# Performance work log

Measured on AMD Instinct MI355X. Metric: run time of the kernel, lower is better.

Reference implementation:

```python
import jax, jax.numpy as jnp
import numpy as np

# Dims (match init_kwargs / input_specs)
B, N, DIM, HEADS, DHEAD, CHUNK = 1, 2048, 1024, 8, 128, 64
HID = 4 * DHEAD            # MemoryMLP expansion_factor=4.0
DI = HEADS * DHEAD         # dim_inner
EPS = 1e-6
MAX_LR = 1.0               # default_step_transform_max_lr


def rmsnorm(x, w):
    return x * jax.lax.rsqrt(jnp.mean(jnp.square(x), -1, keepdims=True) + EPS) * w


def mem_forward(w0, w1, g, x):
    # ResidualNorm(MemoryMLP): y = RMSNorm(gelu(x@w0)@w1)*g + x
    h = jax.nn.gelu(x @ w0, approximate=False) @ w1
    return rmsnorm(h, g) + x


def setup_inputs() -> dict:
    key = jax.random.key(0)
    ks = jax.random.split(key, 12)
    s = lambda i, shape, sc: jax.random.normal(ks[i], shape, jnp.float32) * sc
    return dict(
        x=s(0, (B, N, DIM), 1.0),
        store_norm_w=jnp.ones((DIM,), jnp.float32),
        ret_norm_w=jnp.ones((DIM,), jnp.float32),
        Wq=s(1, (DIM, DI), DIM ** -0.5),
        Wk=s(2, (DIM, DI), DIM ** -0.5),
        Wv=s(3, (DIM, DI), DIM ** -0.5),
        W_step=s(4, (DIM, HEADS), DIM ** -0.5), b_step=jnp.zeros((HEADS,), jnp.float32),
        W_mom=s(5, (DIM, HEADS), DIM ** -0.5), b_mom=jnp.zeros((HEADS,), jnp.float32),
        W_decay=s(6, (DIM, HEADS), DIM ** -0.5), b_decay=jnp.zeros((HEADS,), jnp.float32),
        gate_W=s(7, (DIM, HEADS), DIM ** -0.5),
        combine_W=s(8, (DI, DIM), DI ** -0.5),
        mem_w0=s(9, (HEADS, DHEAD, HID), DHEAD ** -0.5),
        mem_w1=s(10, (HEADS, HID, DHEAD), HID ** -0.5),
        mem_g=jnp.ones((HEADS, DHEAD), jnp.float32),
    )


def reference(x, store_norm_w, ret_norm_w, Wq, Wk, Wv, W_step, b_step,
              W_mom, b_mom, W_decay, b_decay, gate_W, combine_W,
              mem_w0, mem_w1, mem_g):
    b, n, _ = x.shape
    nc = n // CHUNK
    BH = b * HEADS

    # ---- store path ----
    s = rmsnorm(x, store_norm_w)                                 # b n dim
    lr = jax.nn.sigmoid(s @ W_step + b_step) * MAX_LR            # b n h (per-token adaptive step)
    pooled = s.reshape(b, nc, CHUNK, DIM).mean(2)                # b nc dim (AveragePool chunk rep)
    mom = jax.nn.sigmoid(pooled @ W_mom + b_mom)                 # b nc h
    dec = jax.nn.sigmoid(pooled @ W_decay + b_decay)             # b nc h

    def to_chunks(t):  # b n (h d) -> (b h) nc c d
        return t.reshape(b, nc, CHUNK, HEADS, DHEAD).transpose(0, 3, 1, 2, 4).reshape(BH, nc, CHUNK, DHEAD)

    k = to_chunks(s @ Wk)
    v = to_chunks(s @ Wv)
    lr_c = lr.reshape(b, nc, CHUNK, HEADS).transpose(0, 3, 1, 2).reshape(BH, nc, CHUNK)
    mom_bh = mom.transpose(0, 2, 1).reshape(BH, nc)
    dec_bh = dec.transpose(0, 2, 1).reshape(BH, nc)

    # init fast weights per (b h)  (per_head_learned_parameters=True)
    w0 = jnp.broadcast_to(mem_w0[None], (b, HEADS, DHEAD, HID)).reshape(BH, DHEAD, HID)
    w1 = jnp.broadcast_to(mem_w1[None], (b, HEADS, HID, DHEAD)).reshape(BH, HID, DHEAD)
    g = jnp.broadcast_to(mem_g[None], (b, HEADS, DHEAD)).reshape(BH, DHEAD)

    def chunk_loss(w0_, w1_, g_, kc, vc, lrc):
        pred = mem_forward(w0_, w1_, g_, kc)                     # c d
        return jnp.sum(jnp.mean(jnp.square(pred - vc), -1) * lrc)

    grad_chunk = jax.grad(chunk_loss, argnums=(0, 1, 2))
    # vmap over chunks (same weights per chunk, per-sample grads), then over (b h)
    grads = jax.vmap(jax.vmap(grad_chunk, in_axes=(None, None, None, 0, 0, 0)))(w0, w1, g, k, v, lr_c)
    surprises = tuple(-gr for gr in grads)                       # each (BH, nc, ...)

    def combine(a, c):
        ga, xa = a
        gb, xb = c
        return (ga * gb, gb * xa + xb)

    def lin_scan(gates, xs):
        # y_i = gates_i * y_{i-1} + xs_i over chunk axis (axis=1)
        return jax.lax.associative_scan(combine, (gates, xs), axis=1)

    def expand(gates, ref):
        return gates.reshape(gates.shape + (1,) * (ref.ndim - 2))

    # momentum scan per parameter tensor
    updates = tuple(lin_scan(expand(mom_bh, su), su)[1] for su in surprises)

    # weight update scan: W_i = (1 - decay_i) * W_{i-1} + momentum_i, W_{-1} = init
    per_chunk_weights = []
    for upd, w_init in zip(updates, (w0, w1, g)):
        gates = expand(1.0 - dec_bh, upd)
        cumg, y = lin_scan(gates, upd)
        w_seq = y + cumg * w_init[:, None]                       # (BH, nc, ...)
        # retrieval at chunk i uses weights updated through chunk i-1
        per_chunk_weights.append(jnp.concatenate([w_init[:, None], w_seq[:, :-1]], axis=1))
    w0_c, w1_c, g_c = per_chunk_weights

    # ---- retrieve path ----
    r = rmsnorm(x, ret_norm_w)
    q = to_chunks(r @ Wq)                                        # (BH, nc, c, d)
    pred = jax.vmap(jax.vmap(mem_forward))(w0_c, w1_c, g_c, q)   # (BH, nc, c, d)
    out = pred.reshape(b, HEADS, n, DHEAD)                       # b h n d
    gate = jax.nn.sigmoid(r @ gate_W)                            # b n h (retrieve_gate, heads>1)
    out = out * gate.transpose(0, 2, 1)[..., None]
    out = out.transpose(0, 2, 1, 3).reshape(b, n, DI) @ combine_W
    return out
```

## Files before the change

kernel.cpp:

```cpp
#include <hip/hip_runtime.h>
#include <hip/hip_bf16.h>
#include <math.h>

#define NH   8
#define DHD  128
#define HIDN 512
#define CHK  64
#define NCH  32
#define MB   1048576ull

typedef unsigned short u16;
typedef unsigned int   u32;
typedef short s16x8 __attribute__((ext_vector_type(8)));
typedef float f32x4 __attribute__((ext_vector_type(4)));

#define MFMA(a,b,c) __builtin_amdgcn_mfma_f32_16x16x32_bf16((a),(b),(c),0,0,0)

__device__ __forceinline__ float bf2f(u16 v){ return __uint_as_float(((u32)v) << 16); }
__device__ __forceinline__ u16 f2bf(float f){
  u32 u = __float_as_uint(f);
  u += 0x7fffu + ((u >> 16) & 1u);
  return (u16)(u >> 16);
}
__device__ __forceinline__ u32 pack2(float a, float b){
  return (u32)f2bf(a) | ((u32)f2bf(b) << 16);
}
__device__ __forceinline__ float dot2(u32 a, u32 b){
  return __uint_as_float(a << 16)*__uint_as_float(b << 16)
       + __uint_as_float(a & 0xffff0000u)*__uint_as_float(b & 0xffff0000u);
}
__device__ __forceinline__ float waveRedSum(float v){
  #pragma unroll
  for (int off = 32; off; off >>= 1) v += __shfl_xor(v, off);
  return v;
}
__device__ __forceinline__ void gload16(const void* g, void* l){
  __builtin_amdgcn_global_load_lds(
      (const __attribute__((address_space(1))) u32*)g,
      (__attribute__((address_space(3))) u32*)l, 16, 0, 0);
}
__device__ __forceinline__ int swzb(int row, int colb){ return colb ^ ((row & 7) << 4); }
__device__ __forceinline__ int swza(int row, int colb){
  return colb ^ ((row & 7) << 4) ^ (((row >> 3) & 3) << 5);
}



__global__ __launch_bounds__(256) void k_rmsnorm(const float* __restrict__ x,
    const float* __restrict__ wst, const float* __restrict__ wrt,
    u16* __restrict__ s_bf, u16* __restrict__ r_bf){
  int row = blockIdx.x, t = threadIdx.x;
  float4 v = ((const float4*)(x + (size_t)row*1024))[t];
  float ss = v.x*v.x + v.y*v.y + v.z*v.z + v.w*v.w;
  ss = waveRedSum(ss);
  __shared__ float red[4];
  int wv = t >> 6, ln = t & 63;
  if (ln == 0) red[wv] = ss;
  __syncthreads();
  float rr = rsqrtf((red[0]+red[1]+red[2]+red[3])*(1.f/1024.f) + 1e-6f);
  float4 a = ((const float4*)wst)[t];
  float4 b = ((const float4*)wrt)[t];
  uint2 so = make_uint2(pack2(v.x*rr*a.x, v.y*rr*a.y), pack2(v.z*rr*a.z, v.w*rr*a.w));
  uint2 ro = make_uint2(pack2(v.x*rr*b.x, v.y*rr*b.y), pack2(v.z*rr*b.z, v.w*rr*b.w));
  *(uint2*)(s_bf + (size_t)row*1024 + t*4) = so;
  *(uint2*)(r_bf + (size_t)row*1024 + t*4) = ro;
}

__global__ __launch_bounds__(256) void k_pool(const u16* __restrict__ s_bf, float* __restrict__ pooled){
  int c = blockIdx.x; int d = blockIdx.y*256 + threadIdx.x;
  float acc = 0.f;
  for (int tt = 0; tt < 64; ++tt) acc += bf2f(s_bf[((size_t)c*64+tt)*1024 + d]);
  pooled[(size_t)c*1024 + d] = acc * (1.f/64.f);
}

__global__ __launch_bounds__(256) void k_lrgate(const u16* __restrict__ s_bf, const u16* __restrict__ r_bf,
    const u16* __restrict__ WsgL, const float* __restrict__ bstep,
    float* __restrict__ lrc, float* __restrict__ gate){
  int wv = threadIdx.x >> 6, ln = threadIdx.x & 63;
  int tok = blockIdx.x*4 + wv;
  const u16* sp = s_bf + (size_t)tok*1024 + ln*16;
  const u16* rp = r_bf + (size_t)tok*1024 + ln*16;
  uint4 s0 = *(const uint4*)sp, s1 = *(const uint4*)(sp+8);
  uint4 r0 = *(const uint4*)rp, r1 = *(const uint4*)(rp+8);
  #pragma unroll 4
  for (int o = 0; o < 16; ++o){
    const u16* wp = WsgL + (size_t)o*1024 + ln*16;
    uint4 w0v = *(const uint4*)wp, w1v = *(const uint4*)(wp+8);
    uint4 a0 = (o < 8) ? s0 : r0, a1 = (o < 8) ? s1 : r1;
    float acc = dot2(a0.x,w0v.x)+dot2(a0.y,w0v.y)+dot2(a0.z,w0v.z)+dot2(a0.w,w0v.w)
              + dot2(a1.x,w1v.x)+dot2(a1.y,w1v.y)+dot2(a1.z,w1v.z)+dot2(a1.w,w1v.w);
    acc = waveRedSum(acc);
    if (ln == 0){
      int h = o & 7;
      if (o < 8){
        float v = 1.f/(1.f+expf(-(acc + bstep[h])));
        lrc[((size_t)h*NCH + (tok>>6))*CHK + (tok&63)] = v;
      } else {
        gate[(size_t)tok*8 + h] = 1.f/(1.f+expf(-acc));
      }
    }
  }
}

__global__ __launch_bounds__(64) void k_momdec(const float* __restrict__ pooled,
    const float* __restrict__ Wmom, const float* __restrict__ bmom,
    const float* __restrict__ Wdec, const float* __restrict__ bdec,
    float* __restrict__ momb, float* __restrict__ decb){
  int c = blockIdx.x, ln = threadIdx.x;
  const float* prow = pooled + (size_t)c*1024;
  for (int o = 0; o < 16; ++o){
    int h = o & 7;
    const float* W = (o < 8) ? Wmom : Wdec;
    float acc = 0.f;
    for (int k = ln; k < 1024; k += 64) acc += prow[k]*W[(size_t)k*8+h];
    acc = waveRedSum(acc);
    if (ln == 0){
      float bb = (o < 8) ? bmom[h] : bdec[h];
      float v = 1.f/(1.f+expf(-(acc+bb)));
      if (o < 8) momb[h*NCH + c] = v; else decb[h*NCH + c] = v;
    }
  }
}

__global__ __launch_bounds__(256) void k_trf4(
    const float* __restrict__ A0, const float* __restrict__ A1,
    const float* __restrict__ A2, const float* __restrict__ A3,
    u16* __restrict__ O0, u16* __restrict__ O1, u16* __restrict__ O2, u16* __restrict__ O3){
  __shared__ u16 tile[32][34];
  int z = blockIdx.z;
  const float* in = (z==0)?A0:(z==1)?A1:(z==2)?A2:A3;
  u16* out = (z==0)?O0:(z==1)?O1:(z==2)?O2:O3;
  int c0 = blockIdx.x*32, r0 = blockIdx.y*32;
  int tx = threadIdx.x & 31, ty = threadIdx.x >> 5;
  #pragma unroll
  for (int k = 0; k < 4; ++k) tile[ty+k*8][tx] = f2bf(in[(size_t)(r0+ty+k*8)*1024 + c0+tx]);
  __syncthreads();
  #pragma unroll
  for (int k = 0; k < 4; ++k) out[(size_t)(c0+ty+k*8)*1024 + r0+tx] = tile[tx][ty+k*8];
}

__global__ __launch_bounds__(256) void k_packw(const float* __restrict__ mw0, const float* __restrict__ mw1,
    const float* __restrict__ Wstep, const float* __restrict__ gateW,
    u16* __restrict__ w0L, u16* __restrict__ w1L, u16* __restrict__ w1bL, u16* __restrict__ WsgL){
  int h = blockIdx.z, which = blockIdx.y;
  int i = blockIdx.x*256 + threadIdx.x;
  if (which == 3){
    if (h == 0 && i < 16384){
      int o = i >> 10, k = i & 1023;
      float v = (o < 8) ? Wstep[(size_t)k*8 + o] : gateW[(size_t)k*8 + (o-8)];
      WsgL[i] = f2bf(v);
    }
    return;
  }
  int r = i & 511, blk = i >> 9;
  int lg = r >> 7, lr = (r >> 3) & 15, e = r & 7;
  float v; u16* dst;
  if (which == 0){ int n0 = blk >> 2, ks = blk & 3; int hid = n0*16+lr, d = ks*32+lg*8+e;
    v = mw0[(size_t)h*65536 + (size_t)d*512 + hid]; dst = w0L; }
  else if (which == 1){ int n0 = blk >> 4, ks = blk & 15; int d = n0*16+lr, hid = ks*32+lg*8+e;
    v = mw1[(size_t)h*65536 + (size_t)hid*128 + d]; dst = w1L; }
  else { int n0 = blk >> 2, ks = blk & 3; int hid = n0*16+lr, d = ks*32+lg*8+e;
    v = mw1[(size_t)h*65536 + (size_t)hid*128 + d]; dst = w1bL; }
  dst[(size_t)h*65536 + i] = f2bf(v);
}

__device__ __forceinline__ void gemm_body(const u16* __restrict__ A, const u16* __restrict__ BT,
    void* __restrict__ Cp, int mode){
  __shared__ char As[8192];
  __shared__ char Bs[16384];
  int t = threadIdx.x, l = t & 63, w = t >> 6, lr16 = l & 15, lg = l >> 4;
  int wm = w & 1, wn = w >> 1;
  int bm = blockIdx.x*64, bn = blockIdx.y*128;
  f32x4 acc[2][2];
  #pragma unroll
  for (int mt = 0; mt < 2; ++mt)
    #pragma unroll
    for (int nt = 0; nt < 2; ++nt) acc[mt][nt] = (f32x4){0.f,0.f,0.f,0.f};
  for (int k0 = 0; k0 < 1024; k0 += 64){
    gload16(A  + (size_t)(bm + (t>>3))*1024      + k0 + (t&7)*8, As + w*1024);
    gload16(BT + (size_t)(bn + (t>>3))*1024      + k0 + (t&7)*8, Bs + w*1024);
    gload16(BT + (size_t)(bn + 64 + (t>>3))*1024 + k0 + (t&7)*8, Bs + 8192 + w*1024);
    __syncthreads();
    #pragma unroll
    for (int ks = 0; ks < 2; ++ks){
      s16x8 xa[2], yb[2];
      #pragma unroll
      for (int mt = 0; mt < 2; ++mt){ int row = wm*32 + mt*16 + lr16;
        xa[mt] = *(const s16x8*)(As + row*128 + ks*64 + lg*16); }
      #pragma unroll
      for (int nt = 0; nt < 2; ++nt){ int row = wn*32 + nt*16 + lr16;
        yb[nt] = *(const s16x8*)(Bs + row*128 + ks*64 + lg*16); }
      #pragma unroll
      for (int mt = 0; mt < 2; ++mt)
        #pragma unroll
        for (int nt = 0; nt < 2; ++nt) acc[mt][nt] = MFMA(xa[mt], yb[nt], acc[mt][nt]);
    }
    __syncthreads();
  }
  #pragma unroll
  for (int mt = 0; mt < 2; ++mt)
    #pragma unroll
    for (int nt = 0; nt < 2; ++nt)
      #pragma unroll
      for (int j = 0; j < 4; ++j){
        int row = bm + wm*32 + mt*16 + lg*4 + j;
        int coln = bn + wn*32 + nt*16 + lr16;
        if (mode == 0) ((float*)Cp)[(size_t)row*1024 + coln] = acc[mt][nt][j];
        else { int cI = row>>6, tok = row&63, h = coln>>7, d = coln&127;
          ((u16*)Cp)[((size_t)(h*32+cI)*64 + tok)*128 + d] = f2bf(acc[mt][nt][j]); }
      }
}

__global__ __launch_bounds__(512) void k_gemm_bf(const u16* __restrict__ A, const u16* __restrict__ BT,
    void* __restrict__ Cp, int mode){ gemm_body(A, BT, Cp, mode); }

__global__ __launch_bounds__(512) void k_gemm3(
    const u16* __restrict__ s_bf, const u16* __restrict__ r_bf,
    const u16* __restrict__ WkT, const u16* __restrict__ WvT, const u16* __restrict__ WqT,
    u16* __restrict__ Kc, u16* __restrict__ Vc, u16* __restrict__ Qc){
  int z = blockIdx.z;
  const u16* A = (z==2) ? r_bf : s_bf;
  const u16* BT = (z==0) ? WkT : (z==1) ? WvT : WqT;
  u16* C = (z==0) ? Kc : (z==1) ? Vc : Qc;
  gemm_body(A, BT, (void*)C, 1);
}

__global__ __launch_bounds__(512) void k_grad(
    const u16* __restrict__ Kc, const u16* __restrict__ Vc, const float* __restrict__ lrc,
    const u16* __restrict__ w0L, const u16* __restrict__ w1L, const u16* __restrict__ w1bL,
    const float* __restrict__ mg,
    u16* __restrict__ SW0, u16* __restrict__ SW1, float* __restrict__ SG){
  extern __shared__ char sm[];
  char* a_s   = sm;
  char* upT_s = sm + 65536;
  char* dh_s  = sm + 131072;
  char* dhT_s = sm + 147456;
  char* duT_s = a_s;
  char* kcT_s = upT_s;
  char* stg3  = dh_s;
  float* scr  = (float*)dh_s;

  int c = blockIdx.x, bh = blockIdx.y, t = threadIdx.x;
  size_t bc = (size_t)bh*NCH + c;
  int l = t & 63, w = t >> 6, lr16 = l & 15, lg = l >> 4;
  int tg = w & 3, dhf = w >> 2;
  int tokb = tg*16, tok0 = tokb + lg*4;

  const u16* kc_g = Kc + bc*8192;
  const u16* vc_g = Vc + bc*8192;

  s16x8 xk[4];
  #pragma unroll
  for (int k = 0; k < 4; ++k)
    xk[k] = *(const s16x8*)(kc_g + (size_t)(tokb+lr16)*128 + k*32 + lg*8);
  const u16* w0Lh = w0L + (size_t)bh*65536;
  for (int n0h = 0; n0h < 16; ++n0h){
    int n0 = dhf*16 + n0h;
    f32x4 acc = {0.f,0.f,0.f,0.f};
    const u16* yb = w0Lh + (size_t)n0*2048 + l*8;
    #pragma unroll
    for (int k = 0; k < 4; ++k) acc = MFMA(xk[k], *(const s16x8*)(yb + k*512), acc);
    int hid = n0*16 + lr16;
    float upv[4];
    #pragma unroll
    for (int j = 0; j < 4; ++j){
      int tok = tok0 + j;
      float u = acc[j];
      float cdf = 0.5f*(1.f + erff(u*0.70710678118654752f));
      upv[j] = cdf + u*0.3989422804014327f*expf(-0.5f*u*u);
      *(u16*)(a_s + tok*1024 + swza(tok, hid*2)) = f2bf(u*cdf);
    }
    *(uint2*)(upT_s + hid*128 + swzb(hid, tok0*2)) =
        make_uint2(pack2(upv[0], upv[1]), pack2(upv[2], upv[3]));
  }
  __syncthreads();

  s16x8 xa[16];
  #pragma unroll
  for (int k = 0; k < 16; ++k){ int row = tokb + lr16;
    xa[k] = *(const s16x8*)(a_s + row*1024 + swza(row, (k*32+lg*8)*2)); }
  const u16* w1Lh = w1L + (size_t)bh*65536;
  f32x4 hD[4];
  #pragma unroll
  for (int n0l = 0; n0l < 4; ++n0l){
    f32x4 acc = {0.f,0.f,0.f,0.f};
    const u16* yb = w1Lh + (size_t)(dhf*4 + n0l)*8192 + l*8;
    #pragma unroll
    for (int k = 0; k < 16; ++k) acc = MFMA(xa[k], *(const s16x8*)(yb + k*512), acc);
    hD[n0l] = acc;
  }
  #pragma unroll
  for (int j = 0; j < 4; ++j){
    float s = 0.f;
    #pragma unroll
    for (int n0l = 0; n0l < 4; ++n0l) s += hD[n0l][j]*hD[n0l][j];
    s += __shfl_xor(s,1); s += __shfl_xor(s,2); s += __shfl_xor(s,4); s += __shfl_xor(s,8);
    if (lr16 == 0) scr[dhf*64 + tok0 + j] = s;
  }
  __syncthreads();
  float rv[4], lrv[4], dotp[4];
  #pragma unroll
  for (int j = 0; j < 4; ++j){
    int tok = tok0 + j;
    float tot = scr[tok] + scr[64 + tok];
    rv[j] = rsqrtf(tot*(1.f/128.f) + 1e-6f);
    lrv[j] = lrc[bc*64 + tok];
    dotp[j] = 0.f;
  }
  float dn[4][4];
  #pragma unroll
  for (int n0l = 0; n0l < 4; ++n0l){
    int d = dhf*64 + n0l*16 + lr16;
    float g0 = mg[(size_t)bh*128 + d];
    float dgav = 0.f;
    #pragma unroll
    for (int j = 0; j < 4; ++j){
      int tok = tok0 + j;
      float h = hD[n0l][j];
      float nrm = h*rv[j];
      float kcv = bf2f(kc_g[(size_t)tok*128 + d]);
      float vcv = bf2f(vc_g[(size_t)tok*128 + d]);
      float p = nrm*g0 + kcv;
      float dp = (2.f/128.f)*lrv[j]*(p - vcv);
      dgav += dp*nrm;
      float dnv = dp*g0;
      dn[n0l][j] = dnv;
      dotp[j] += dnv*h;
    }
    dgav += __shfl_xor(dgav,16); dgav += __shfl_xor(dgav,32);
    if (lg == 0) scr[256 + w*64 + n0l*16 + lr16] = dgav;
  }
  #pragma unroll
  for (int j = 0; j < 4; ++j){
    float dd = dotp[j];
    dd += __shfl_xor(dd,1); dd += __shfl_xor(dd,2); dd += __shfl_xor(dd,4); dd += __shfl_xor(dd,8);
    if (lr16 == 0) scr[128 + dhf*64 + tok0 + j] = dd;
  }
  __syncthreads();
  float dotv[4];
  #pragma unroll
  for (int j = 0; j < 4; ++j){
    int tok = tok0 + j;
    dotv[j] = scr[128 + tok] + scr[128 + 64 + tok];
  }
  if (t < 128){
    int dh2 = t >> 6, dl = t & 63;
    float s = scr[256 + (dh2*4+0)*64 + dl] + scr[256 + (dh2*4+1)*64 + dl]
            + scr[256 + (dh2*4+2)*64 + dl] + scr[256 + (dh2*4+3)*64 + dl];
    SG[bc*128 + t] = -s;
  }
  __syncthreads();
  #pragma unroll
  for (int n0l = 0; n0l < 4; ++n0l){
    int d = dhf*64 + n0l*16 + lr16;
    float dhv[4];
    #pragma unroll
    for (int j = 0; j < 4; ++j){
      int tok = tok0 + j;
      float c3 = rv[j]*rv[j]*rv[j]*(1.f/128.f);
      dhv[j] = rv[j]*dn[n0l][j] - c3*dotv[j]*hD[n0l][j];
      *(u16*)(dh_s + tok*256 + swzb(tok, d*2)) = f2bf(dhv[j]);
    }
    *(uint2*)(dhT_s + d*128 + swzb(d, tok0*2)) =
        make_uint2(pack2(dhv[0], dhv[1]), pack2(dhv[2], dhv[3]));
  }
  __syncthreads();

  {
    s16x8 yB[4][2];
    #pragma unroll
    for (int n0l = 0; n0l < 4; ++n0l){
      int hid = w*64 + n0l*16 + lr16;
      #pragma unroll
      for (int ks = 0; ks < 2; ++ks){
        s16x8 v;
        #pragma unroll
        for (int e = 0; e < 8; ++e){ int tok = ks*32 + lg*8 + e;
          v[e] = *(const short*)(a_s + tok*1024 + swza(tok, hid*2)); }
        yB[n0l][ks] = v;
      }
    }
    __syncthreads();
    u16* stg = (u16*)(a_s + w*8192);
    #pragma unroll 1
    for (int half = 0; half < 2; ++half){
      #pragma unroll
      for (int mt4 = 0; mt4 < 4; ++mt4){
        int mt = half*4 + mt4; int row = mt*16 + lr16;
        s16x8 xD0 = *(const s16x8*)(dhT_s + row*128 + swzb(row, (lg*8)*2));
        s16x8 xD1 = *(const s16x8*)(dhT_s + row*128 + swzb(row, (32+lg*8)*2));
        #pragma unroll
        for (int n0l = 0; n0l < 4; ++n0l){
          f32x4 acc = {0.f,0.f,0.f,0.f};
          acc = MFMA(xD0, yB[n0l][0], acc);
          acc = MFMA(xD1, yB[n0l][1], acc);
          int base = mt4*1024 + (n0l>>1)*512 + (((n0l*2)+(lr16>>3))&3)*128 + (lr16&7);
          #pragma unroll
          for (int j = 0; j < 4; ++j)
            stg[base + (lg*4+j)*8] = f2bf(-acc[j]);
        }
      }
      asm volatile("s_waitcnt lgkmcnt(0)" ::: "memory");
      #pragma unroll
      for (int mt4 = 0; mt4 < 4; ++mt4){
        int mt = half*4 + mt4;
        u16* gb = SW1 + bc*65536 + (size_t)(mt*16 + w*2)*512;
        s16x8 o0 = *(const s16x8*)(stg + mt4*1024 + l*16);
        s16x8 o1 = *(const s16x8*)(stg + mt4*1024 + l*16 + 8);
        *(s16x8*)(gb + l*16) = o0;
        *(s16x8*)(gb + l*16 + 8) = o1;
      }
    }
  }
  __syncthreads();

  {
    s16x8 xDh[4][4];
    #pragma unroll
    for (int mt = 0; mt < 4; ++mt){ int row = mt*16 + lr16;
      #pragma unroll
      for (int ks = 0; ks < 4; ++ks)
        xDh[mt][ks] = *(const s16x8*)(dh_s + row*256 + swzb(row, (ks*32+lg*8)*2)); }
    const u16* w1bh = w1bL + (size_t)bh*65536;
    #pragma unroll 2
    for (int n0l = 0; n0l < 4; ++n0l){
      int hid = w*64 + n0l*16 + lr16;
      s16x8 yW[4];
      const u16* xb = w1bh + (size_t)(w*4 + n0l)*2048 + l*8;
      #pragma unroll
      for (int ks = 0; ks < 4; ++ks)
        yW[ks] = *(const s16x8*)(xb + ks*512);
      #pragma unroll
      for (int mt = 0; mt < 4; ++mt){
        f32x4 acc = {0.f,0.f,0.f,0.f};
        #pragma unroll
        for (int ks = 0; ks < 4; ++ks) acc = MFMA(xDh[mt][ks], yW[ks], acc);
        int tk0 = mt*16 + lg*4;
        uint2 ur = *(const uint2*)(upT_s + hid*128 + swzb(hid, tk0*2));
        float u0 = bf2f((u16)(ur.x & 0xffff)), u1 = bf2f((u16)(ur.x >> 16));
        float u2 = bf2f((u16)(ur.y & 0xffff)), u3 = bf2f((u16)(ur.y >> 16));
        *(uint2*)(duT_s + hid*128 + swzb(hid, tk0*2)) =
            make_uint2(pack2(acc[0]*u0, acc[1]*u1), pack2(acc[2]*u2, acc[3]*u3));
      }
    }
  }
  __syncthreads();

  #pragma unroll
  for (int i = 0; i < 2; ++i){
    int idx = i*512 + t;
    int tok = idx & 63, d0 = (idx >> 6)*8;
    s16x8 kv = *(const s16x8*)(kc_g + (size_t)tok*128 + d0);
    #pragma unroll
    for (int e = 0; e < 8; ++e)
      *(u16*)(kcT_s + (d0+e)*128 + swzb(d0+e, tok*2)) = kv[e];
  }
  __syncthreads();

  {
    s16x8 yK[8][2];
    #pragma unroll
    for (int n0 = 0; n0 < 8; ++n0){
      int d = n0*16 + lr16;
      #pragma unroll
      for (int ks = 0; ks < 2; ++ks)
        yK[n0][ks] = *(const s16x8*)(kcT_s + d*128 + swzb(d, (ks*32+lg*8)*2));
    }
    u16* stg = (u16*)(stg3 + w*4096);
    #pragma unroll 1
    for (int mi = 0; mi < 4; ++mi){
      int hid = w*64 + mi*16 + lr16;
      s16x8 xU0 = *(const s16x8*)(duT_s + hid*128 + swzb(hid, (lg*8)*2));
      s16x8 xU1 = *(const s16x8*)(duT_s + hid*128 + swzb(hid, (32+lg*8)*2));
      #pragma unroll
      for (int n0 = 0; n0 < 8; ++n0){
        f32x4 acc = {0.f,0.f,0.f,0.f};
        acc = MFMA(xU0, yK[n0][0], acc);
        acc = MFMA(xU1, yK[n0][1], acc);
        int base = (n0>>1)*512 + (((n0*2)+(lr16>>3))&3)*128 + (lr16&7);
        #pragma unroll
        for (int j = 0; j < 4; ++j)
          stg[base + (lg*4+j)*8] = f2bf(-acc[j]);
      }
      asm volatile("s_waitcnt lgkmcnt(0)" ::: "memory");
      u16* gb = SW0 + bc*65536 + (size_t)(w*4 + mi)*2048;
      #pragma unroll
      for (int q = 0; q < 4; ++q){
        s16x8 o = *(const s16x8*)(stg + l*32 + q*8);
        *(s16x8*)(gb + l*32 + q*8) = o;
      }
    }
  }
}

__global__ __launch_bounds__(256) void k_scan(
    const u16* __restrict__ w0L, const u16* __restrict__ w1L, const float* __restrict__ mg,
    const u16* __restrict__ SW0, const u16* __restrict__ SW1, const float* __restrict__ SG,
    const float* __restrict__ momb, const float* __restrict__ decb,
    u16* __restrict__ W0C, u16* __restrict__ W1C, float* __restrict__ GC){
  int bh = blockIdx.y;
  int e = blockIdx.x*256 + threadIdx.x;
  const float* momp = momb + bh*NCH;
  const float* decp = decb + bh*NCH;
  float m = 0.f, Wv;
  if (e < 65536){
    Wv = bf2f(w0L[(size_t)bh*65536 + e]);
    const u16* su = SW0 + (size_t)bh*NCH*65536 + e;
    u16* outp = W0C + (size_t)bh*NCH*65536 + e;
    for (int c = 0; c < NCH; ++c){
      outp[(size_t)c*65536] = f2bf(Wv);
      m = momp[c]*m + bf2f(su[(size_t)c*65536]);
      Wv = (1.f - decp[c])*Wv + m;
    }
  } else if (e < 131072){
    int e2 = e - 65536;
    Wv = bf2f(w1L[(size_t)bh*65536 + e2]);
    const u16* su = SW1 + (size_t)bh*NCH*65536 + e2;
    u16* outp = W1C + (size_t)bh*NCH*65536 + e2;
    for (int c = 0; c < NCH; ++c){
      outp[(size_t)c*65536] = f2bf(Wv);
      m = momp[c]*m + bf2f(su[(size_t)c*65536]);
      Wv = (1.f - decp[c])*Wv + m;
    }
  } else if (e < 131200){
    int e3 = e - 131072;
    Wv = mg[(size_t)bh*128 + e3];
    const float* su = SG + (size_t)bh*NCH*128 + e3;
    float* outp = GC + (size_t)bh*NCH*128 + e3;
    for (int c = 0; c < NCH; ++c){
      outp[(size_t)c*128] = Wv;
      m = momp[c]*m + su[(size_t)c*128];
      Wv = (1.f - decp[c])*Wv + m;
    }
  }
}

__global__ __launch_bounds__(512) void k_retr(
    const u16* __restrict__ Qc, const u16* __restrict__ W0C, const u16* __restrict__ W1C,
    const float* __restrict__ GC, const float* __restrict__ gate, u16* __restrict__ OH){
  extern __shared__ char sm[];
  char* a_s = sm;
  float* scr = (float*)(sm + 65536);
  int c = blockIdx.x, bh = blockIdx.y, t = threadIdx.x;
  size_t bc = (size_t)bh*NCH + c;
  int l = t & 63, w = t >> 6, lr16 = l & 15, lg = l >> 4;
  int tg = w & 3, dhf = w >> 2;
  const u16* q_g = Qc + bc*8192;

  s16x8 xq[4];
  #pragma unroll
  for (int k = 0; k < 4; ++k)
    xq[k] = *(const s16x8*)(q_g + (size_t)(tg*16+lr16)*128 + k*32 + lg*8);
  const u16* w0c = W0C + bc*65536;
  for (int n0h = 0; n0h < 16; ++n0h){
    int n0 = dhf*16 + n0h;
    f32x4 acc = {0.f,0.f,0.f,0.f};
    const u16* yb = w0c + (size_t)n0*2048 + l*8;
    #pragma unroll
    for (int k = 0; k < 4; ++k) acc = MFMA(xq[k], *(const s16x8*)(yb + k*512), acc);
    int hid = n0*16 + lr16;
    #pragma unroll
    for (int j = 0; j < 4; ++j){
      int tok = tg*16 + lg*4 + j;
      float u = acc[j];
      float av = u*0.5f*(1.f + erff(u*0.70710678118654752f));
      *(u16*)(a_s + tok*1024 + swza(tok, hid*2)) = f2bf(av);
    }
  }
  __syncthreads();
  s16x8 xa[16];
  #pragma unroll
  for (int k = 0; k < 16; ++k){ int row = tg*16 + lr16;
    xa[k] = *(const s16x8*)(a_s + row*1024 + swza(row, (k*32+lg*8)*2)); }
  const u16* w1c = W1C + bc*65536;
  f32x4 hD[4];
  #pragma unroll
  for (int n0l = 0; n0l < 4; ++n0l){
    f32x4 acc = {0.f,0.f,0.f,0.f};
    const u16* yb = w1c + (size_t)(dhf*4 + n0l)*8192 + l*8;
    #pragma unroll
    for (int k = 0; k < 16; ++k) acc = MFMA(xa[k], *(const s16x8*)(yb + k*512), acc);
    hD[n0l] = acc;
  }
  #pragma unroll
  for (int j = 0; j < 4; ++j){
    float s = 0.f;
    #pragma unroll
    for (int n0l = 0; n0l < 4; ++n0l) s += hD[n0l][j]*hD[n0l][j];
    s += __shfl_xor(s,1); s += __shfl_xor(s,2); s += __shfl_xor(s,4); s += __shfl_xor(s,8);
    if (lr16 == 0) scr[dhf*64 + tg*16 + lg*4 + j] = s;
  }
  __syncthreads();
  float rv[4], gtv[4];
  #pragma unroll
  for (int j = 0; j < 4; ++j){
    int tok = tg*16 + lg*4 + j;
    rv[j] = rsqrtf((scr[tok] + scr[64 + tok])*(1.f/128.f) + 1e-6f);
    gtv[j] = gate[(size_t)(c*64 + tok)*8 + bh];
  }
  #pragma unroll
  for (int n0l = 0; n0l < 4; ++n0l){
    int d = dhf*64 + n0l*16 + lr16;
    float g0 = GC[bc*128 + d];
    #pragma unroll
    for (int j = 0; j < 4; ++j){
      int tok = tg*16 + lg*4 + j; int tokg = c*64 + tok;
      float qv = bf2f(q_g[(size_t)tok*128 + d]);
      float p = hD[n0l][j]*rv[j]*g0 + qv;
      OH[(size_t)tokg*1024 + bh*128 + d] = f2bf(p*gtv[j]);
    }
  }
}

extern "C" void kernel_launch(void* const* d_in, const int* in_sizes, int n_in,
                              void* d_out, int out_size, void* d_ws, size_t ws_size,
                              hipStream_t stream) {
  (void)in_sizes; (void)n_in; (void)out_size; (void)ws_size;
  const float* x     = (const float*)d_in[0];
  const float* snw   = (const float*)d_in[1];
  const float* rnw   = (const float*)d_in[2];
  const float* Wq    = (const float*)d_in[3];
  const float* Wk    = (const float*)d_in[4];
  const float* Wv    = (const float*)d_in[5];
  const float* Wstep = (const float*)d_in[6];
  const float* bstep = (const float*)d_in[7];
  const float* Wmom  = (const float*)d_in[8];
  const float* bmom  = (const float*)d_in[9];
  const float* Wdec  = (const float*)d_in[10];
  const float* bdec  = (const float*)d_in[11];
  const float* gateW = (const float*)d_in[12];
  const float* combW = (const float*)d_in[13];
  const float* mw0   = (const float*)d_in[14];
  const float* mw1   = (const float*)d_in[15];
  const float* mg    = (const float*)d_in[16];
  float* out = (float*)d_out;

  char* Wb = (char*)d_ws;
  u16* Qc    = (u16*)(Wb + 0*MB);
  u16* Kc    = (u16*)(Wb + 4*MB);
  u16* Vc    = (u16*)(Wb + 8*MB);
  u16* s_bf  = (u16*)(Wb + 12*MB);
  u16* r_bf  = (u16*)(Wb + 16*MB);
  u16* WqT   = (u16*)(Wb + 20*MB);
  u16* WkT   = (u16*)(Wb + 22*MB);
  u16* WvT   = (u16*)(Wb + 24*MB);
  u16* combT = (u16*)(Wb + 26*MB);
  u16* w0L   = (u16*)(Wb + 28*MB);
  u16* w1L   = (u16*)(Wb + 29*MB);
  u16* w1bL  = (u16*)(Wb + 30*MB);
  u16* OH    = (u16*)(Wb + 31*MB);
  u16* SW0   = (u16*)(Wb + 35*MB);
  u16* SW1   = (u16*)(Wb + 67*MB);
  u16* W0C   = (u16*)(Wb + 99*MB);
  u16* W1C   = (u16*)(Wb + 131*MB);
  float* pooled = (float*)(Wb + 163*MB);
  float* lrc    = (float*)(Wb + 163*MB + 131072);
  float* momb   = (float*)(Wb + 163*MB + 196608);
  float* decb   = (float*)(Wb + 163*MB + 197632);
  float* gate   = (float*)(Wb + 163*MB + 198656);
  float* SG     = (float*)(Wb + 163*MB + 264192);
  float* GC     = (float*)(Wb + 163*MB + 395264);
  u16* WsgL  = (u16*)(Wb + 163*MB + 526336);

  hipFuncSetAttribute((const void*)k_grad, hipFuncAttributeMaxDynamicSharedMemorySize, 163840);
  hipFuncSetAttribute((const void*)k_retr, hipFuncAttributeMaxDynamicSharedMemorySize, 66560);

  k_rmsnorm<<<2048, 256, 0, stream>>>(x, snw, rnw, s_bf, r_bf);
  k_pool<<<dim3(32,4), 256, 0, stream>>>(s_bf, pooled);
  k_packw<<<dim3(256,4,8), 256, 0, stream>>>(mw0, mw1, Wstep, gateW, w0L, w1L, w1bL, WsgL);
  k_lrgate<<<512, 256, 0, stream>>>(s_bf, r_bf, WsgL, bstep, lrc, gate);
  k_momdec<<<32, 64, 0, stream>>>(pooled, Wmom, bmom, Wdec, bdec, momb, decb);
  k_trf4<<<dim3(32,32,4), 256, 0, stream>>>(Wq, Wk, Wv, combW, WqT, WkT, WvT, combT);
  k_gemm3<<<dim3(32,8,3), 512, 0, stream>>>(s_bf, r_bf, WkT, WvT, WqT, Kc, Vc, Qc);
  k_grad<<<dim3(32,8), 512, 163840, stream>>>(Kc, Vc, lrc, w0L, w1L, w1bL, mg, SW0, SW1, SG);
  k_scan<<<dim3(513,8), 256, 0, stream>>>(w0L, w1L, mg, SW0, SW1, SG, momb, decb, W0C, W1C, GC);
  k_retr<<<dim3(32,8), 512, 66560, stream>>>(Qc, W0C, W1C, GC, gate, OH);
  k_gemm_bf<<<dim3(32,8), 512, 0, stream>>>(OH, combT, (void*)out, 0);
}
```

Baseline: 228.3 us.

## Fuse lr/gate and mom/decay kernels, tanh GELU, batch weight loads in grad/retr

Merges the lr/gate and momentum/decay projection kernels into one launch. Swaps the exact erf GELU and its derivative for a tanh approximation using fast exp. Batches global weight loads ahead of the MFMA chains in k_grad and k_retr, prefetches the key and value elements earlier, and adds launch-bounds occupancy hints. Also restages the SW0 output through reused LDS in two halves. The tanh GELU differs slightly from the reference's exact GELU, and the extra registers held by the batched loads could lower occupancy.

```diff
diff --git a/kernel.cpp b/kernel.cpp
--- a/kernel.cpp
+++ b/kernel.cpp
@@ -33,6 +33,15 @@
   #pragma unroll
   for (int off = 32; off; off >>= 1) v += __shfl_xor(v, off);
   return v;
+}
+__device__ __forceinline__ float gelu_v(float u, float& t){
+  float g = 0.7978845608f*(u + 0.044715f*u*u*u);
+  float e = __expf(2.f*g);
+  t = 1.f - __fdividef(2.f, e + 1.f);
+  return 0.5f*u*(1.f + t);
+}
+__device__ __forceinline__ float gelu_d(float u, float t){
+  return 0.5f*(1.f + t) + 0.5f*u*(1.f - t*t)*0.7978845608f*(1.f + 0.134145f*u*u);
 }
 __device__ __forceinline__ void gload16(const void* g, void* l){
   __builtin_amdgcn_global_load_lds(
@@ -73,51 +82,54 @@
   pooled[(size_t)c*1024 + d] = acc * (1.f/64.f);
 }
 
-__global__ __launch_bounds__(256) void k_lrgate(const u16* __restrict__ s_bf, const u16* __restrict__ r_bf,
+__global__ __launch_bounds__(256) void k_lrmd(const u16* __restrict__ s_bf, const u16* __restrict__ r_bf,
     const u16* __restrict__ WsgL, const float* __restrict__ bstep,
-    float* __restrict__ lrc, float* __restrict__ gate){
-  int wv = threadIdx.x >> 6, ln = threadIdx.x & 63;
-  int tok = blockIdx.x*4 + wv;
-  const u16* sp = s_bf + (size_t)tok*1024 + ln*16;
-  const u16* rp = r_bf + (size_t)tok*1024 + ln*16;
-  uint4 s0 = *(const uint4*)sp, s1 = *(const uint4*)(sp+8);
-  uint4 r0 = *(const uint4*)rp, r1 = *(const uint4*)(rp+8);
-  #pragma unroll 4
-  for (int o = 0; o < 16; ++o){
-    const u16* wp = WsgL + (size_t)o*1024 + ln*16;
-    uint4 w0v = *(const uint4*)wp, w1v = *(const uint4*)(wp+8);
-    uint4 a0 = (o < 8) ? s0 : r0, a1 = (o < 8) ? s1 : r1;
-    float acc = dot2(a0.x,w0v.x)+dot2(a0.y,w0v.y)+dot2(a0.z,w0v.z)+dot2(a0.w,w0v.w)
-              + dot2(a1.x,w1v.x)+dot2(a1.y,w1v.y)+dot2(a1.z,w1v.z)+dot2(a1.w,w1v.w);
-    acc = waveRedSum(acc);
-    if (ln == 0){
-      int h = o & 7;
-      if (o < 8){
-        float v = 1.f/(1.f+expf(-(acc + bstep[h])));
-        lrc[((size_t)h*NCH + (tok>>6))*CHK + (tok&63)] = v;
-      } else {
-        gate[(size_t)tok*8 + h] = 1.f/(1.f+expf(-acc));
-      }
-    }
-  }
-}
-
-__global__ __launch_bounds__(64) void k_momdec(const float* __restrict__ pooled,
+    const float* __restrict__ pooled,
     const float* __restrict__ Wmom, const float* __restrict__ bmom,
     const float* __restrict__ Wdec, const float* __restrict__ bdec,
+    float* __restrict__ lrc, float* __restrict__ gate,
     float* __restrict__ momb, float* __restrict__ decb){
-  int c = blockIdx.x, ln = threadIdx.x;
-  const float* prow = pooled + (size_t)c*1024;
-  for (int o = 0; o < 16; ++o){
-    int h = o & 7;
-    const float* W = (o < 8) ? Wmom : Wdec;
-    float acc = 0.f;
-    for (int k = ln; k < 1024; k += 64) acc += prow[k]*W[(size_t)k*8+h];
-    acc = waveRedSum(acc);
-    if (ln == 0){
-      float bb = (o < 8) ? bmom[h] : bdec[h];
-      float v = 1.f/(1.f+expf(-(acc+bb)));
-      if (o < 8) momb[h*NCH + c] = v; else decb[h*NCH + c] = v;
+  int bx = blockIdx.x;
+  if (bx < 512){
+    int wv = threadIdx.x >> 6, ln = threadIdx.x & 63;
+    int tok = bx*4 + wv;
+    const u16* sp = s_bf + (size_t)tok*1024 + ln*16;
+    const u16* rp = r_bf + (size_t)tok*1024 + ln*16;
+    uint4 s0 = *(const uint4*)sp, s1 = *(const uint4*)(sp+8);
+    uint4 r0 = *(const uint4*)rp, r1 = *(const uint4*)(rp+8);
+    #pragma unroll 4
+    for (int o = 0; o < 16; ++o){
+      const u16* wp = WsgL + (size_t)o*1024 + ln*16;
+      uint4 w0v = *(const uint4*)wp, w1v = *(const uint4*)(wp+8);
+      uint4 a0 = (o < 8) ? s0 : r0, a1 = (o < 8) ? s1 : r1;
+      float acc = dot2(a0.x,w0v.x)+dot2(a0.y,w0v.y)+dot2(a0.z,w0v.z)+dot2(a0.w,w0v.w)
+                + dot2(a1.x,w1v.x)+dot2(a1.y,w1v.y)+dot2(a1.z,w1v.z)+dot2(a1.w,w1v.w);
+      acc = waveRedSum(acc);
+      if (ln == 0){
+        int h = o & 7;
+        if (o < 8){
+          float v = 1.f/(1.f+expf(-(acc + bstep[h])));
+          lrc[((size_t)h*NCH + (tok>>6))*CHK + (tok&63)] = v;
+        } else {
+          gate[(size_t)tok*8 + h] = 1.f/(1.f+expf(-acc));
+        }
+      }
+    }
+  } else {
+    if (threadIdx.x >= 64) return;
+    int c = bx - 512, ln = threadIdx.x;
+    const float* prow = pooled + (size_t)c*1024;
+    for (int o = 0; o < 16; ++o){
+      int h = o & 7;
+      const float* W = (o < 8) ? Wmom : Wdec;
+      float acc = 0.f;
+      for (int k = ln; k < 1024; k += 64) acc += prow[k]*W[(size_t)k*8+h];
+      acc = waveRedSum(acc);
+      if (ln == 0){
+        float bb = (o < 8) ? bmom[h] : bdec[h];
+        float v = 1.f/(1.f+expf(-(acc+bb)));
+        if (o < 8) momb[h*NCH + c] = v; else decb[h*NCH + c] = v;
+      }
     }
   }
 }
@@ -225,7 +237,7 @@
   gemm_body(A, BT, (void*)C, 1);
 }
 
-__global__ __launch_bounds__(512) void k_grad(
+__global__ __launch_bounds__(512, 2) void k_grad(
     const u16* __restrict__ Kc, const u16* __restrict__ Vc, const float* __restrict__ lrc,
     const u16* __restrict__ w0L, const u16* __restrict__ w1L, const u16* __restrict__ w1bL,
     const float* __restrict__ mg,
@@ -237,7 +249,6 @@
   char* dhT_s = sm + 147456;
   char* duT_s = a_s;
   char* kcT_s = upT_s;
-  char* stg3  = dh_s;
   float* scr  = (float*)dh_s;
 
   int c = blockIdx.x, bh = blockIdx.y, t = threadIdx.x;
@@ -251,27 +262,37 @@
 
   s16x8 xk[4];
   #pragma unroll
-  for (int k = 0; k < 4; ++k)
-    xk[k] = *(const s16x8*)(kc_g + (size_t)(tokb+lr16)*128 + k*32 + lg*8);
+  for (int ks = 0; ks < 4; ++ks)
+    xk[ks] = *(const s16x8*)(kc_g + (size_t)(tokb+lr16)*128 + ks*32 + lg*8);
   const u16* w0Lh = w0L + (size_t)bh*65536;
-  for (int n0h = 0; n0h < 16; ++n0h){
-    int n0 = dhf*16 + n0h;
-    f32x4 acc = {0.f,0.f,0.f,0.f};
-    const u16* yb = w0Lh + (size_t)n0*2048 + l*8;
-    #pragma unroll
-    for (int k = 0; k < 4; ++k) acc = MFMA(xk[k], *(const s16x8*)(yb + k*512), acc);
-    int hid = n0*16 + lr16;
-    float upv[4];
-    #pragma unroll
-    for (int j = 0; j < 4; ++j){
-      int tok = tok0 + j;
-      float u = acc[j];
-      float cdf = 0.5f*(1.f + erff(u*0.70710678118654752f));
-      upv[j] = cdf + u*0.3989422804014327f*expf(-0.5f*u*u);
-      *(u16*)(a_s + tok*1024 + swza(tok, hid*2)) = f2bf(u*cdf);
-    }
-    *(uint2*)(upT_s + hid*128 + swzb(hid, tok0*2)) =
-        make_uint2(pack2(upv[0], upv[1]), pack2(upv[2], upv[3]));
+  #pragma unroll
+  for (int gq = 0; gq < 4; ++gq){
+    s16x8 yb[4][4];
+    #pragma unroll
+    for (int q = 0; q < 4; ++q){
+      const u16* p = w0Lh + (size_t)(dhf*16 + gq*4 + q)*2048 + l*8;
+      #pragma unroll
+      for (int ks = 0; ks < 4; ++ks) yb[q][ks] = *(const s16x8*)(p + ks*512);
+    }
+    #pragma unroll
+    for (int q = 0; q < 4; ++q){
+      int n0 = dhf*16 + gq*4 + q;
+      f32x4 acc = {0.f,0.f,0.f,0.f};
+      #pragma unroll
+      for (int ks = 0; ks < 4; ++ks) acc = MFMA(xk[ks], yb[q][ks], acc);
+      int hid = n0*16 + lr16;
+      float upv[4];
+      #pragma unroll
+      for (int j = 0; j < 4; ++j){
+        int tok = tok0 + j;
+        float u = acc[j], tt;
+        float av = gelu_v(u, tt);
+        upv[j] = gelu_d(u, tt);
+        *(u16*)(a_s + tok*1024 + swza(tok, hid*2)) = f2bf(av);
+      }
+      *(uint2*)(upT_s + hid*128 + swzb(hid, tok0*2)) =
+          make_uint2(pack2(upv[0], upv[1]), pack2(upv[2], upv[3]));
+    }
   }
   __syncthreads();
 
@@ -279,14 +300,27 @@
   #pragma unroll
   for (int k = 0; k < 16; ++k){ int row = tokb + lr16;
     xa[k] = *(const s16x8*)(a_s + row*1024 + swza(row, (k*32+lg*8)*2)); }
+  float kcv[4][4], vcv[4][4];
+  #pragma unroll
+  for (int n0l = 0; n0l < 4; ++n0l){
+    int d = dhf*64 + n0l*16 + lr16;
+    #pragma unroll
+    for (int j = 0; j < 4; ++j){
+      kcv[n0l][j] = bf2f(kc_g[(size_t)(tok0+j)*128 + d]);
+      vcv[n0l][j] = bf2f(vc_g[(size_t)(tok0+j)*128 + d]);
+    }
+  }
   const u16* w1Lh = w1L + (size_t)bh*65536;
   f32x4 hD[4];
   #pragma unroll
   for (int n0l = 0; n0l < 4; ++n0l){
+    s16x8 yw[16];
+    #pragma unroll
+    for (int k = 0; k < 16; ++k)
+      yw[k] = *(const s16x8*)(w1Lh + (size_t)(dhf*4 + n0l)*8192 + l*8 + (size_t)k*512);
     f32x4 acc = {0.f,0.f,0.f,0.f};
-    const u16* yb = w1Lh + (size_t)(dhf*4 + n0l)*8192 + l*8;
-    #pragma unroll
-    for (int k = 0; k < 16; ++k) acc = MFMA(xa[k], *(const s16x8*)(yb + k*512), acc);
+    #pragma unroll
+    for (int k = 0; k < 16; ++k) acc = MFMA(xa[k], yw[k], acc);
     hD[n0l] = acc;
   }
   #pragma unroll
@@ -315,13 +349,10 @@
     float dgav = 0.f;
     #pragma unroll
     for (int j = 0; j < 4; ++j){
-      int tok = tok0 + j;
       float h = hD[n0l][j];
       float nrm = h*rv[j];
-      float kcv = bf2f(kc_g[(size_t)tok*128 + d]);
-      float vcv = bf2f(vc_g[(size_t)tok*128 + d]);
-      float p = nrm*g0 + kcv;
-      float dp = (2.f/128.f)*lrv[j]*(p - vcv);
+      float p = nrm*g0 + kcv[n0l][j];
+      float dp = (2.f/128.f)*lrv[j]*(p - vcv[n0l][j]);
       dgav += dp*nrm;
       float dnv = dp*g0;
       dn[n0l][j] = dnv;
@@ -466,28 +497,31 @@
       for (int ks = 0; ks < 2; ++ks)
         yK[n0][ks] = *(const s16x8*)(kcT_s + d*128 + swzb(d, (ks*32+lg*8)*2));
     }
-    u16* stg = (u16*)(stg3 + w*4096);
     #pragma unroll 1
     for (int mi = 0; mi < 4; ++mi){
       int hid = w*64 + mi*16 + lr16;
       s16x8 xU0 = *(const s16x8*)(duT_s + hid*128 + swzb(hid, (lg*8)*2));
       s16x8 xU1 = *(const s16x8*)(duT_s + hid*128 + swzb(hid, (32+lg*8)*2));
-      #pragma unroll
-      for (int n0 = 0; n0 < 8; ++n0){
-        f32x4 acc = {0.f,0.f,0.f,0.f};
-        acc = MFMA(xU0, yK[n0][0], acc);
-        acc = MFMA(xU1, yK[n0][1], acc);
-        int base = (n0>>1)*512 + (((n0*2)+(lr16>>3))&3)*128 + (lr16&7);
+      u16* stgw = (u16*)(duT_s + (size_t)(w*64 + mi*16)*128);
+      u16* gb = SW0 + bc*65536 + (size_t)(w*4 + mi)*2048;
+      #pragma unroll 1
+      for (int hh = 0; hh < 2; ++hh){
         #pragma unroll
-        for (int j = 0; j < 4; ++j)
-          stg[base + (lg*4+j)*8] = f2bf(-acc[j]);
-      }
-      asm volatile("s_waitcnt lgkmcnt(0)" ::: "memory");
-      u16* gb = SW0 + bc*65536 + (size_t)(w*4 + mi)*2048;
-      #pragma unroll
-      for (int q = 0; q < 4; ++q){
-        s16x8 o = *(const s16x8*)(stg + l*32 + q*8);
-        *(s16x8*)(gb + l*32 + q*8) = o;
+        for (int n0h = 0; n0h < 4; ++n0h){
+          int n0 = hh*4 + n0h;
+          f32x4 acc = {0.f,0.f,0.f,0.f};
+          acc = MFMA(xU0, yK[n0][0], acc);
+          acc = MFMA(xU1, yK[n0][1], acc);
+          int base = (n0h>>1)*512 + (((n0h*2)+(lr16>>3))&3)*128 + (lr16&7);
+          #pragma unroll
+          for (int j = 0; j < 4; ++j)
+            stgw[base + (lg*4+j)*8] = f2bf(-acc[j]);
+        }
+        asm volatile("s_waitcnt lgkmcnt(0)" ::: "memory");
+        s16x8 o0 = *(const s16x8*)(stgw + l*16);
+        s16x8 o1 = *(const s16x8*)(stgw + l*16 + 8);
+        *(s16x8*)(gb + hh*1024 + l*16) = o0;
+        *(s16x8*)(gb + hh*1024 + l*16 + 8) = o1;
       }
     }
   }
@@ -535,7 +569,7 @@
   }
 }
 
-__global__ __launch_bounds__(512) void k_retr(
+__global__ __launch_bounds__(512, 4) void k_retr(
     const u16* __restrict__ Qc, const u16* __restrict__ W0C, const u16* __restrict__ W1C,
     const float* __restrict__ GC, const float* __restrict__ gate, u16* __restrict__ OH){
   extern __shared__ char sm[];
@@ -545,41 +579,59 @@
   size_t bc = (size_t)bh*NCH + c;
   int l = t & 63, w = t >> 6, lr16 = l & 15, lg = l >> 4;
   int tg = w & 3, dhf = w >> 2;
+  int tokb = tg*16, tok0 = tokb + lg*4;
   const u16* q_g = Qc + bc*8192;
 
   s16x8 xq[4];
   #pragma unroll
   for (int k = 0; k < 4; ++k)
-    xq[k] = *(const s16x8*)(q_g + (size_t)(tg*16+lr16)*128 + k*32 + lg*8);
+    xq[k] = *(const s16x8*)(q_g + (size_t)(tokb+lr16)*128 + k*32 + lg*8);
   const u16* w0c = W0C + bc*65536;
-  for (int n0h = 0; n0h < 16; ++n0h){
-    int n0 = dhf*16 + n0h;
-    f32x4 acc = {0.f,0.f,0.f,0.f};
-    const u16* yb = w0c + (size_t)n0*2048 + l*8;
-    #pragma unroll
-    for (int k = 0; k < 4; ++k) acc = MFMA(xq[k], *(const s16x8*)(yb + k*512), acc);
-    int hid = n0*16 + lr16;
-    #pragma unroll
-    for (int j = 0; j < 4; ++j){
-      int tok = tg*16 + lg*4 + j;
-      float u = acc[j];
-      float av = u*0.5f*(1.f + erff(u*0.70710678118654752f));
-      *(u16*)(a_s + tok*1024 + swza(tok, hid*2)) = f2bf(av);
+  #pragma unroll
+  for (int gq = 0; gq < 4; ++gq){
+    s16x8 yb[4][4];
+    #pragma unroll
+    for (int q = 0; q < 4; ++q){
+      const u16* p = w0c + (size_t)(dhf*16 + gq*4 + q)*2048 + l*8;
+      #pragma unroll
+      for (int ks = 0; ks < 4; ++ks) yb[q][ks] = *(const s16x8*)(p + ks*512);
+    }
+    #pragma unroll
+    for (int q = 0; q < 4; ++q){
+      int n0 = dhf*16 + gq*4 + q;
+      f32x4 acc = {0.f,0.f,0.f,0.f};
+      #pragma unroll
+      for (int ks = 0; ks < 4; ++ks) acc = MFMA(xq[ks], yb[q][ks], acc);
+      int hid = n0*16 + lr16;
+      #pragma unroll
+      for (int j = 0; j < 4; ++j){
+        int tok = tok0 + j;
+        float u = acc[j], tt;
+        float av = gelu_v(u, tt);
+        *(u16*)(a_s + tok*1024 + swza(tok, hid*2)) = f2bf(av);
+      }
     }
   }
   __syncthreads();
   s16x8 xa[16];
   #pragma unroll
-  for (int k = 0; k < 16; ++k){ int row = tg*16 + lr16;
+  for (int k = 0; k < 16; ++k){ int row = tokb + lr16;
     xa[k] = *(const s16x8*)(a_s + row*1024 + swza(row, (k*32+lg*8)*2)); }
   const u16* w1c = W1C + bc*65536;
   f32x4 hD[4];
   #pragma unroll
   for (int n0l = 0; n0l < 4; ++n0l){
+    const u16* yb = w1c + (size_t)(dhf*4 + n0l)*8192 + l*8;
     f32x4 acc = {0.f,0.f,0.f,0.f};
-    const u16* yb = w1c + (size_t)(dhf*4 + n0l)*8192 + l*8;
-    #pragma unroll
-    for (int k = 0; k < 16; ++k) acc = MFMA(xa[k], *(const s16x8*)(yb + k*512), acc);
+    #pragma unroll
+    for (int kb = 0; kb < 4; ++kb){
+      s16x8 yw[4];
+      #pragma unroll
+      for (int kk = 0; kk < 4; ++kk)
+        yw[kk] = *(const s16x8*)(yb + (size_t)(kb*4+kk)*512);
+      #pragma unroll
+      for (int kk = 0; kk < 4; ++kk) acc = MFMA(xa[kb*4+kk], yw[kk], acc);
+    }
     hD[n0l] = acc;
   }
   #pragma unroll
@@ -588,13 +640,13 @@
     #pragma unroll
     for (int n0l = 0; n0l < 4; ++n0l) s += hD[n0l][j]*hD[n0l][j];
     s += __shfl_xor(s,1); s += __shfl_xor(s,2); s += __shfl_xor(s,4); s += __shfl_xor(s,8);
-    if (lr16 == 0) scr[dhf*64 + tg*16 + lg*4 + j] = s;
+    if (lr16 == 0) scr[dhf*64 + tok0 + j] = s;
   }
   __syncthreads();
   float rv[4], gtv[4];
   #pragma unroll
   for (int j = 0; j < 4; ++j){
-    int tok = tg*16 + lg*4 + j;
+    int tok = tok0 + j;
     rv[j] = rsqrtf((scr[tok] + scr[64 + tok])*(1.f/128.f) + 1e-6f);
     gtv[j] = gate[(size_t)(c*64 + tok)*8 + bh];
   }
@@ -604,7 +656,7 @@
     float g0 = GC[bc*128 + d];
     #pragma unroll
     for (int j = 0; j < 4; ++j){
-      int tok = tg*16 + lg*4 + j; int tokg = c*64 + tok;
+      int tok = tok0 + j; int tokg = c*64 + tok;
       float qv = bf2f(q_g[(size_t)tok*128 + d]);
       float p = hD[n0l][j]*rv[j]*g0 + qv;
       OH[(size_t)tokg*1024 + bh*128 + d] = f2bf(p*gtv[j]);
@@ -668,8 +720,8 @@
   k_rmsnorm<<<2048, 256, 0, stream>>>(x, snw, rnw, s_bf, r_bf);
   k_pool<<<dim3(32,4), 256, 0, stream>>>(s_bf, pooled);
   k_packw<<<dim3(256,4,8), 256, 0, stream>>>(mw0, mw1, Wstep, gateW, w0L, w1L, w1bL, WsgL);
-  k_lrgate<<<512, 256, 0, stream>>>(s_bf, r_bf, WsgL, bstep, lrc, gate);
-  k_momdec<<<32, 64, 0, stream>>>(pooled, Wmom, bmom, Wdec, bdec, momb, decb);
+  k_lrmd<<<544, 256, 0, stream>>>(s_bf, r_bf, WsgL, bstep, pooled, Wmom, bmom, Wdec, bdec,
+                                  lrc, gate, momb, decb);
   k_trf4<<<dim3(32,32,4), 256, 0, stream>>>(Wq, Wk, Wv, combW, WqT, WkT, WvT, combT);
   k_gemm3<<<dim3(32,8,3), 512, 0, stream>>>(s_bf, r_bf, WkT, WvT, WqT, Kc, Vc, Qc);
   k_grad<<<dim3(32,8), 512, 163840, stream>>>(Kc, Vc, lrc, w0L, w1L, w1bL, mg, SW0, SW1, SG);
```

New measurement: 229.6 us. Within noise of the previous version (+0.6%).
